# Kernel tuning notes

Hardware: AMD Instinct MI355X
Metric: run time of the kernel (lower is better)

Reference implementation:

```python
import jax, jax.numpy as jnp
import numpy as np

SOS_INDEX = 0


def setup_inputs() -> dict:
    key = jax.random.key(0)
    ks = jax.random.split(key, 12)
    T, B, H, V = 64, 1024, 512, 512
    s = 1.0 / np.sqrt(H)
    inp = {
        "target_var": jax.random.randint(ks[0], (T, B), 0, V, dtype=jnp.int64),
        "target_max_len": T,
        "encoder_hidden": jax.random.normal(ks[1], (B, H), jnp.float32),
        "encoder_cell": jax.random.normal(ks[2], (B, H), jnp.float32),
        "embedding": jax.random.normal(ks[3], (V, H), jnp.float32) * s,
        "W_ih": jax.random.normal(ks[4], (4 * H, H), jnp.float32) * s,
        "W_hh": jax.random.normal(ks[5], (4 * H, H), jnp.float32) * s,
        "b_ih": jax.random.normal(ks[6], (4 * H,), jnp.float32) * s,
        "b_hh": jax.random.normal(ks[7], (4 * H,), jnp.float32) * s,
        "W_out": jax.random.normal(ks[8], (V, H), jnp.float32) * s,
        "b_out": jax.random.normal(ks[9], (V,), jnp.float32) * s,
    }
    return inp


def reference(target_var, target_max_len, encoder_hidden, encoder_cell,
              embedding, W_ih, W_hh, b_ih, b_hh, W_out, b_out):
    B = target_var.shape[1]
    H = encoder_hidden.shape[1]
    # initial decoder input: embedding of SOS token for every batch element
    x0 = jnp.broadcast_to(embedding[SOS_INDEX], (B, H))
    bias = b_ih + b_hh  # [4H]

    def step(carry, _):
        x, h, c = carry
        # PyTorch LSTMCell: gate order i, f, g, o
        gates = x @ W_ih.T + h @ W_hh.T + bias  # [B, 4H]
        i, f, g, o = jnp.split(gates, 4, axis=-1)
        c_new = jax.nn.sigmoid(f) * c + jax.nn.sigmoid(i) * jnp.tanh(g)
        h_new = jax.nn.sigmoid(o) * jnp.tanh(c_new)
        logits = h_new @ W_out.T + b_out  # [B, V]
        # greedy decoding (topk(1)) -> next input embedding
        nxt = embedding[jnp.argmax(logits, axis=-1)]  # [B, H]
        return (nxt, h_new, c_new), logits

    _, outputs = jax.lax.scan(step, (x0, encoder_hidden, encoder_cell),
                              None, length=target_max_len)
    return outputs  # [T, B, V]
```

## Files before the change

kernel.cpp:

```cpp
#include <hip/hip_runtime.h>
#include <math.h>

constexpr int T_STEPS = 64;
constexpr int B_SZ = 1024;
constexpr int H_SZ = 512;
constexpr int V_SZ = 512;
constexpr int G_SZ = 4 * H_SZ;

typedef _Float16 half8 __attribute__((ext_vector_type(8)));
typedef _Float16 half4 __attribute__((ext_vector_type(4)));
typedef float f32x4 __attribute__((ext_vector_type(4)));

__device__ __forceinline__ float4 ld4(const float* p) {
    return *reinterpret_cast<const float4*>(p);
}
__device__ __forceinline__ void st4(float* p, float4 v) {
    *reinterpret_cast<float4*>(p) = v;
}
__device__ __forceinline__ float sigf(float x) { return 1.f / (1.f + expf(-x)); }

__device__ __forceinline__ unsigned long long pack_vc(float v, int col) {
    unsigned u = __float_as_uint(v);
    unsigned key = (u & 0x80000000u) ? ~u : (u | 0x80000000u);
    return ((unsigned long long)key << 32) | (unsigned)(511 - col);
}

__global__ __launch_bounds__(256) void cvt_pair(
    const float* __restrict__ x, _Float16* __restrict__ hi,
    _Float16* __restrict__ lo)
{
    const int i4 = blockIdx.x * 256 + threadIdx.x;
    const float4 v = ld4(x + (size_t)i4 * 4);
    half4 h, l;
    const float h0 = (float)(_Float16)v.x; h[0] = (_Float16)v.x; l[0] = (_Float16)((v.x - h0) * 2048.f);
    const float h1 = (float)(_Float16)v.y; h[1] = (_Float16)v.y; l[1] = (_Float16)((v.y - h1) * 2048.f);
    const float h2 = (float)(_Float16)v.z; h[2] = (_Float16)v.z; l[2] = (_Float16)((v.z - h2) * 2048.f);
    const float h3 = (float)(_Float16)v.w; h[3] = (_Float16)v.w; l[3] = (_Float16)((v.w - h3) * 2048.f);
    *reinterpret_cast<half4*>(hi + (size_t)i4 * 4) = h;
    *reinterpret_cast<half4*>(lo + (size_t)i4 * 4) = l;
}

__global__ __launch_bounds__(256) void gemm_nt_f32(
    const float* __restrict__ A, const float* __restrict__ Bw,
    float* __restrict__ C, int M, int N, int K,
    const float* __restrict__ bias1, const float* __restrict__ bias2)
{
    constexpr int BK = 16;
    __shared__ __align__(16) float As[BK][64];
    __shared__ __align__(16) float Bs[BK][64];
    const int tid = threadIdx.x;
    const int tx = tid % 16, ty = tid / 16;
    const int m0 = blockIdx.y * 64, n0 = blockIdx.x * 64;
    const int lr = tid / 4, lc = (tid % 4) * 4;
    float acc[4][4] = {};
    for (int k0 = 0; k0 < K; k0 += BK) {
        const float4 av = ld4(&A[(size_t)(m0 + lr) * K + (k0 + lc)]);
        const float4 bv = ld4(&Bw[(size_t)(n0 + lr) * K + (k0 + lc)]);
        __syncthreads();
        As[lc + 0][lr] = av.x; As[lc + 1][lr] = av.y; As[lc + 2][lr] = av.z; As[lc + 3][lr] = av.w;
        Bs[lc + 0][lr] = bv.x; Bs[lc + 1][lr] = bv.y; Bs[lc + 2][lr] = bv.z; Bs[lc + 3][lr] = bv.w;
        __syncthreads();
#pragma unroll
        for (int k = 0; k < BK; ++k) {
            const float4 a4 = ld4(&As[k][ty * 4]);
            const float4 b4 = ld4(&Bs[k][tx * 4]);
            const float ar[4] = {a4.x, a4.y, a4.z, a4.w};
            const float br[4] = {b4.x, b4.y, b4.z, b4.w};
#pragma unroll
            for (int i = 0; i < 4; ++i)
#pragma unroll
                for (int j = 0; j < 4; ++j)
                    acc[i][j] = fmaf(ar[i], br[j], acc[i][j]);
        }
    }
    const int nc = n0 + tx * 4;
    const float4 b1 = ld4(&bias1[nc]);
    const float4 b2 = ld4(&bias2[nc]);
#pragma unroll
    for (int i = 0; i < 4; ++i) {
        const int m = m0 + ty * 4 + i;
        float4 v;
        v.x = acc[i][0] + b1.x + b2.x; v.y = acc[i][1] + b1.y + b2.y;
        v.z = acc[i][2] + b1.z + b2.z; v.w = acc[i][3] + b1.w + b2.w;
        st4(&C[(size_t)m * N + nc], v);
    }
}

__global__ __launch_bounds__(256) void step_gates_cell(
    const _Float16* __restrict__ Ahi, const _Float16* __restrict__ Alo,
    const _Float16* __restrict__ Whh_hi, const _Float16* __restrict__ Whh_lo,
    const float* __restrict__ Eg,
    const unsigned long long* __restrict__ tok_cur,
    unsigned long long* __restrict__ tok_reset,
    float* __restrict__ cbuf,
    _Float16* __restrict__ Nhi, _Float16* __restrict__ Nlo)
{
    constexpr int LDK = 40;
    __shared__ __align__(16) char smem[64 * 129 * 4];
    _Float16* sAh = (_Float16*)smem;
    _Float16* sAl = sAh + 64 * LDK;
    _Float16* sBh = sAl + 64 * LDK;
    _Float16* sBl = sBh + 128 * LDK;
    float* sg = (float*)smem;

    const int tid = threadIdx.x;
    const int wave = tid >> 6, lane = tid & 63;
    const int wm = wave >> 1, wn = wave & 1;
    const int lm = lane & 15, kq = lane >> 4;
    const int h0 = blockIdx.x * 32;
    const int b0 = blockIdx.y * 64;

    const int ar = tid >> 2, akc = (tid & 3) * 8;
    const int r1 = tid >> 2, kc1 = (tid & 3) * 8;
    const int r2 = (tid + 256) >> 2, kc2 = kc1;
    const int g1 = (r1 >> 5) * 512 + h0 + (r1 & 31);
    const int g2 = (r2 >> 5) * 512 + h0 + (r2 & 31);

    const _Float16* pAh = Ahi + (size_t)(b0 + ar) * 512 + akc;
    const _Float16* pAl = Alo + (size_t)(b0 + ar) * 512 + akc;
    const _Float16* pB1h = Whh_hi + (size_t)g1 * 512 + kc1;
    const _Float16* pB1l = Whh_lo + (size_t)g1 * 512 + kc1;
    const _Float16* pB2h = Whh_hi + (size_t)g2 * 512 + kc2;
    const _Float16* pB2l = Whh_lo + (size_t)g2 * 512 + kc2;

    f32x4 aH[2][4] = {};
    f32x4 aC[2][4] = {};

    for (int k0 = 0; k0 < 512; k0 += 32) {
        const half8 va_h = *(const half8*)(pAh + k0);
        const half8 va_l = *(const half8*)(pAl + k0);
        const half8 vb1h = *(const half8*)(pB1h + k0);
        const half8 vb1l = *(const half8*)(pB1l + k0);
        const half8 vb2h = *(const half8*)(pB2h + k0);
        const half8 vb2l = *(const half8*)(pB2l + k0);
        __syncthreads();
        *(half8*)(sAh + ar * LDK + akc) = va_h;
        *(half8*)(sAl + ar * LDK + akc) = va_l;
        *(half8*)(sBh + r1 * LDK + kc1) = vb1h;
        *(half8*)(sBl + r1 * LDK + kc1) = vb1l;
        *(half8*)(sBh + r2 * LDK + kc2) = vb2h;
        *(half8*)(sBl + r2 * LDK + kc2) = vb2l;
        __syncthreads();

        half8 bh[4], bl[4];
#pragma unroll
        for (int gn = 0; gn < 4; ++gn) {
            const int rr = wn * 64 + gn * 16 + lm;
            bh[gn] = *(const half8*)(sBh + rr * LDK + kq * 8);
            bl[gn] = *(const half8*)(sBl + rr * LDK + kq * 8);
        }
#pragma unroll
        for (int gm = 0; gm < 2; ++gm) {
            const int rm = wm * 32 + gm * 16 + lm;
            const half8 ah = *(const half8*)(sAh + rm * LDK + kq * 8);
            const half8 al = *(const half8*)(sAl + rm * LDK + kq * 8);
#pragma unroll
            for (int gn = 0; gn < 4; ++gn)
                aH[gm][gn] = __builtin_amdgcn_mfma_f32_16x16x32_f16(ah, bh[gn], aH[gm][gn], 0, 0, 0);
#pragma unroll
            for (int gn = 0; gn < 4; ++gn)
                aC[gm][gn] = __builtin_amdgcn_mfma_f32_16x16x32_f16(ah, bl[gn], aC[gm][gn], 0, 0, 0);
#pragma unroll
            for (int gn = 0; gn < 4; ++gn)
                aC[gm][gn] = __builtin_amdgcn_mfma_f32_16x16x32_f16(al, bh[gn], aC[gm][gn], 0, 0, 0);
        }
    }

    __syncthreads();
#pragma unroll
    for (int gm = 0; gm < 2; ++gm) {
#pragma unroll
        for (int gn = 0; gn < 4; ++gn) {
            const int row = wm * 32 + gm * 16 + kq * 4;
            const int col = wn * 64 + gn * 16 + lm;
#pragma unroll
            for (int r = 0; r < 4; ++r)
                sg[(row + r) * 129 + col] =
                    aH[gm][gn][r] + aC[gm][gn][r] * (1.f / 2048.f);
        }
    }
    __syncthreads();

    const int crow = tid >> 2;
    const int hb = (tid & 3) * 8;
    const int b = b0 + crow;
    const unsigned long long pk = tok_cur[b];
    const int tk = 511 - (int)(unsigned)(pk & 0xFFFFFFFFu);
    const float* egp = Eg + (size_t)tk * G_SZ + h0;

#pragma unroll
    for (int q = 0; q < 2; ++q) {
        const int hh = hb + q * 4;
        const float* sr = sg + crow * 129;
        const float4 gI = ld4(sr + hh);
        const float4 gF = ld4(sr + 32 + hh);
        const float4 gG = ld4(sr + 64 + hh);
        const float4 gO = ld4(sr + 96 + hh);
        const float4 eI = ld4(egp + hh);
        const float4 eF = ld4(egp + 512 + hh);
        const float4 eG = ld4(egp + 1024 + hh);
        const float4 eO = ld4(egp + 1536 + hh);
        const size_t ci = (size_t)b * 512 + h0 + hh;
        const float4 cv = ld4(cbuf + ci);

        const float iv[4] = {gI.x + eI.x, gI.y + eI.y, gI.z + eI.z, gI.w + eI.w};
        const float fv[4] = {gF.x + eF.x, gF.y + eF.y, gF.z + eF.z, gF.w + eF.w};
        const float gv[4] = {gG.x + eG.x, gG.y + eG.y, gG.z + eG.z, gG.w + eG.w};
        const float ov[4] = {gO.x + eO.x, gO.y + eO.y, gO.z + eO.z, gO.w + eO.w};
        float cc[4] = {cv.x, cv.y, cv.z, cv.w};
        float hn[4];
#pragma unroll
        for (int j = 0; j < 4; ++j) {
            const float cn = sigf(fv[j]) * cc[j] + sigf(iv[j]) * tanhf(gv[j]);
            cc[j] = cn;
            hn[j] = sigf(ov[j]) * tanhf(cn);
        }
        st4(cbuf + ci, make_float4(cc[0], cc[1], cc[2], cc[3]));
        half4 h, l;
#pragma unroll
        for (int j = 0; j < 4; ++j) {
            const _Float16 hi = (_Float16)hn[j];
            h[j] = hi;
            l[j] = (_Float16)((hn[j] - (float)hi) * 2048.f);
        }
        *reinterpret_cast<half4*>(Nhi + ci) = h;
        *reinterpret_cast<half4*>(Nlo + ci) = l;
    }

    if (blockIdx.x == 0 && tid < 64) tok_reset[b0 + tid] = 0ULL;
}

__global__ __launch_bounds__(128) void step_logits_argmax(
    const _Float16* __restrict__ Ahi, const _Float16* __restrict__ Alo,
    const _Float16* __restrict__ Whi, const _Float16* __restrict__ Wlo,
    const float* __restrict__ b_out,
    float* __restrict__ outT,
    unsigned long long* __restrict__ tokmax)
{
    const int tid = threadIdx.x, wave = tid >> 6, lane = tid & 63;
    const int lm = lane & 15, kq = lane >> 4;
    const int n0 = blockIdx.x * 64;
    const int m0 = blockIdx.y * 32 + wave * 16;

    f32x4 aH[4] = {};
    f32x4 aC[4] = {};

    const _Float16* pAh = Ahi + (size_t)(m0 + lm) * 512 + kq * 8;
    const _Float16* pAl = Alo + (size_t)(m0 + lm) * 512 + kq * 8;

    for (int k0 = 0; k0 < 512; k0 += 32) {
        const half8 ah = *(const half8*)(pAh + k0);
        const half8 al = *(const half8*)(pAl + k0);
        half8 bh[4], bl[4];
#pragma unroll
        for (int gn = 0; gn < 4; ++gn) {
            const size_t off = (size_t)(n0 + gn * 16 + lm) * 512 + k0 + kq * 8;
            bh[gn] = *(const half8*)(Whi + off);
            bl[gn] = *(const half8*)(Wlo + off);
        }
#pragma unroll
        for (int gn = 0; gn < 4; ++gn)
            aH[gn] = __builtin_amdgcn_mfma_f32_16x16x32_f16(ah, bh[gn], aH[gn], 0, 0, 0);
#pragma unroll
        for (int gn = 0; gn < 4; ++gn)
            aC[gn] = __builtin_amdgcn_mfma_f32_16x16x32_f16(ah, bl[gn], aC[gn], 0, 0, 0);
#pragma unroll
        for (int gn = 0; gn < 4; ++gn)
            aC[gn] = __builtin_amdgcn_mfma_f32_16x16x32_f16(al, bh[gn], aC[gn], 0, 0, 0);
    }

    unsigned long long best[4] = {0ULL, 0ULL, 0ULL, 0ULL};
#pragma unroll
    for (int gn = 0; gn < 4; ++gn) {
        const int col = n0 + gn * 16 + lm;
        const float bo = b_out[col];
#pragma unroll
        for (int r = 0; r < 4; ++r) {
            const float v = aH[gn][r] + aC[gn][r] * (1.f / 2048.f) + bo;
            const int row = m0 + kq * 4 + r;
            outT[(size_t)row * V_SZ + col] = v;
            const unsigned long long p = pack_vc(v, col);
            if (p > best[r]) best[r] = p;
        }
    }
#pragma unroll
    for (int r = 0; r < 4; ++r) {
#pragma unroll
        for (int off = 1; off < 16; off <<= 1) {
            const unsigned long long o = __shfl_xor(best[r], off);
            if (o > best[r]) best[r] = o;
        }
    }
    if (lm == 0) {
#pragma unroll
        for (int r = 0; r < 4; ++r)
            atomicMax(&tokmax[m0 + kq * 4 + r], best[r]);
    }
}

__global__ __launch_bounds__(256) void init_tok(unsigned long long* __restrict__ tok)
{
    const int i = blockIdx.x * 256 + threadIdx.x;
    tok[i] = (i < 1024) ? 511ULL : 0ULL;
}

extern "C" void kernel_launch(void* const* d_in, const int* in_sizes, int n_in,
                              void* d_out, int out_size, void* d_ws, size_t ws_size,
                              hipStream_t stream)
{
    const float* enc_h = (const float*)d_in[2];
    const float* enc_c = (const float*)d_in[3];
    const float* emb   = (const float*)d_in[4];
    const float* W_ih  = (const float*)d_in[5];
    const float* W_hh  = (const float*)d_in[6];
    const float* b_ih  = (const float*)d_in[7];
    const float* b_hh  = (const float*)d_in[8];
    const float* W_out = (const float*)d_in[9];
    const float* b_out = (const float*)d_in[10];
    float* out = (float*)d_out;

    char* ws = (char*)d_ws;
    _Float16* Whh_hi  = (_Float16*)(ws);
    _Float16* Whh_lo  = (_Float16*)(ws + (2u << 20));
    _Float16* Wout_hi = (_Float16*)(ws + (4u << 20));
    _Float16* Wout_lo = (_Float16*)(ws + (4u << 20) + (512u << 10));
    _Float16* Hhi[2] = {(_Float16*)(ws + (5u << 20)), (_Float16*)(ws + (7u << 20))};
    _Float16* Hlo[2] = {(_Float16*)(ws + (6u << 20)), (_Float16*)(ws + (8u << 20))};
    float* cbuf = (float*)(ws + (9u << 20));
    float* Eg   = (float*)(ws + (11u << 20));
    unsigned long long* tokbuf = (unsigned long long*)(ws + (15u << 20));

    const dim3 blk256(256), blk128(128);

    cvt_pair<<<(G_SZ * H_SZ) / 1024, blk256, 0, stream>>>(W_hh, Whh_hi, Whh_lo);
    cvt_pair<<<(V_SZ * H_SZ) / 1024, blk256, 0, stream>>>(W_out, Wout_hi, Wout_lo);
    cvt_pair<<<(B_SZ * H_SZ) / 1024, blk256, 0, stream>>>(enc_h, Hhi[0], Hlo[0]);
    hipMemcpyAsync(cbuf, enc_c, (size_t)B_SZ * H_SZ * 4, hipMemcpyDeviceToDevice, stream);
    init_tok<<<8, blk256, 0, stream>>>(tokbuf);

    gemm_nt_f32<<<dim3(G_SZ / 64, V_SZ / 64), blk256, 0, stream>>>(
        emb, W_ih, Eg, V_SZ, G_SZ, H_SZ, b_ih, b_hh);

    for (int t = 0; t < T_STEPS; ++t) {
        const int cur = t & 1, nxt = (t + 1) & 1;
        step_gates_cell<<<dim3(H_SZ / 32, B_SZ / 64), blk256, 0, stream>>>(
            Hhi[cur], Hlo[cur], Whh_hi, Whh_lo, Eg,
            tokbuf + cur * B_SZ, tokbuf + nxt * B_SZ,
            cbuf, Hhi[nxt], Hlo[nxt]);

        step_logits_argmax<<<dim3(V_SZ / 64, B_SZ / 32), blk128, 0, stream>>>(
            Hhi[nxt], Hlo[nxt], Wout_hi, Wout_lo, b_out,
            out + (size_t)t * B_SZ * V_SZ, tokbuf + nxt * B_SZ);
    }
}
```

Baseline: 2.302 ms.

## Fuse per-step decoder kernels into one persistent kernel with grid barriers

```diff
diff --git a/kernel.cpp b/kernel.cpp
--- a/kernel.cpp
+++ b/kernel.cpp
@@ -6,6 +6,7 @@
 constexpr int H_SZ = 512;
 constexpr int V_SZ = 512;
 constexpr int G_SZ = 4 * H_SZ;
+constexpr int N_BLOCKS = 256;
 
 typedef _Float16 half8 __attribute__((ext_vector_type(8)));
 typedef _Float16 half4 __attribute__((ext_vector_type(4)));
@@ -23,6 +24,27 @@
     unsigned u = __float_as_uint(v);
     unsigned key = (u & 0x80000000u) ? ~u : (u | 0x80000000u);
     return ((unsigned long long)key << 32) | (unsigned)(511 - col);
+}
+
+__device__ __forceinline__ void grid_barrier(unsigned* cnt, unsigned* gen) {
+    __syncthreads();
+    if (threadIdx.x == 0) {
+        const unsigned g = __hip_atomic_load(gen, __ATOMIC_RELAXED,
+                                             __HIP_MEMORY_SCOPE_AGENT);
+        const unsigned arrived = __hip_atomic_fetch_add(
+            cnt, 1u, __ATOMIC_ACQ_REL, __HIP_MEMORY_SCOPE_AGENT) + 1u;
+        if (arrived == (unsigned)N_BLOCKS) {
+            __hip_atomic_store(cnt, 0u, __ATOMIC_RELAXED,
+                               __HIP_MEMORY_SCOPE_AGENT);
+            __hip_atomic_fetch_add(gen, 1u, __ATOMIC_RELEASE,
+                                   __HIP_MEMORY_SCOPE_AGENT);
+        } else {
+            while (__hip_atomic_load(gen, __ATOMIC_ACQUIRE,
+                                     __HIP_MEMORY_SCOPE_AGENT) == g)
+                __builtin_amdgcn_s_sleep(2);
+        }
+    }
+    __syncthreads();
 }
 
 __global__ __launch_bounds__(256) void cvt_pair(
@@ -86,14 +108,22 @@
     }
 }
 
-__global__ __launch_bounds__(256) void step_gates_cell(
-    const _Float16* __restrict__ Ahi, const _Float16* __restrict__ Alo,
+__global__ __launch_bounds__(256) void init_state(
+    unsigned long long* __restrict__ tok, unsigned* __restrict__ bar)
+{
+    const int i = blockIdx.x * 256 + threadIdx.x;
+    tok[i] = (i < 1024) ? 511ULL : 0ULL;
+    if (i < 2) bar[i] = 0u;
+}
+
+__global__ __launch_bounds__(256, 1) void persistent_decoder(
     const _Float16* __restrict__ Whh_hi, const _Float16* __restrict__ Whh_lo,
-    const float* __restrict__ Eg,
-    const unsigned long long* __restrict__ tok_cur,
-    unsigned long long* __restrict__ tok_reset,
-    float* __restrict__ cbuf,
-    _Float16* __restrict__ Nhi, _Float16* __restrict__ Nlo)
+    const _Float16* __restrict__ Wout_hi, const _Float16* __restrict__ Wout_lo,
+    const float* __restrict__ Eg, const float* __restrict__ b_out,
+    _Float16* __restrict__ H0hi, _Float16* __restrict__ H0lo,
+    _Float16* __restrict__ H1hi, _Float16* __restrict__ H1lo,
+    float* __restrict__ cbuf, unsigned long long* __restrict__ tokbuf,
+    unsigned* __restrict__ bar, float* __restrict__ out)
 {
     constexpr int LDK = 40;
     __shared__ __align__(16) char smem[64 * 129 * 4];
@@ -103,205 +133,215 @@
     _Float16* sBl = sBh + 128 * LDK;
     float* sg = (float*)smem;
 
+    unsigned* bar_cnt = bar;
+    unsigned* bar_gen = bar + 1;
+
+    const int bid = blockIdx.x;
     const int tid = threadIdx.x;
     const int wave = tid >> 6, lane = tid & 63;
+    const int lm = lane & 15, kq = lane >> 4;
+
     const int wm = wave >> 1, wn = wave & 1;
-    const int lm = lane & 15, kq = lane >> 4;
-    const int h0 = blockIdx.x * 32;
-    const int b0 = blockIdx.y * 64;
-
+    const int h0 = (bid & 15) * 32;
+    const int b0 = (bid >> 4) * 64;
     const int ar = tid >> 2, akc = (tid & 3) * 8;
-    const int r1 = tid >> 2, kc1 = (tid & 3) * 8;
-    const int r2 = (tid + 256) >> 2, kc2 = kc1;
-    const int g1 = (r1 >> 5) * 512 + h0 + (r1 & 31);
+    const int r2 = ar + 64;
+    const int g1 = (ar >> 5) * 512 + h0 + (ar & 31);
     const int g2 = (r2 >> 5) * 512 + h0 + (r2 & 31);
-
-    const _Float16* pAh = Ahi + (size_t)(b0 + ar) * 512 + akc;
-    const _Float16* pAl = Alo + (size_t)(b0 + ar) * 512 + akc;
-    const _Float16* pB1h = Whh_hi + (size_t)g1 * 512 + kc1;
-    const _Float16* pB1l = Whh_lo + (size_t)g1 * 512 + kc1;
-    const _Float16* pB2h = Whh_hi + (size_t)g2 * 512 + kc2;
-    const _Float16* pB2l = Whh_lo + (size_t)g2 * 512 + kc2;
-
-    f32x4 aH[2][4] = {};
-    f32x4 aC[2][4] = {};
-
-    for (int k0 = 0; k0 < 512; k0 += 32) {
-        const half8 va_h = *(const half8*)(pAh + k0);
-        const half8 va_l = *(const half8*)(pAl + k0);
-        const half8 vb1h = *(const half8*)(pB1h + k0);
-        const half8 vb1l = *(const half8*)(pB1l + k0);
-        const half8 vb2h = *(const half8*)(pB2h + k0);
-        const half8 vb2l = *(const half8*)(pB2l + k0);
-        __syncthreads();
-        *(half8*)(sAh + ar * LDK + akc) = va_h;
-        *(half8*)(sAl + ar * LDK + akc) = va_l;
-        *(half8*)(sBh + r1 * LDK + kc1) = vb1h;
-        *(half8*)(sBl + r1 * LDK + kc1) = vb1l;
-        *(half8*)(sBh + r2 * LDK + kc2) = vb2h;
-        *(half8*)(sBl + r2 * LDK + kc2) = vb2l;
-        __syncthreads();
-
-        half8 bh[4], bl[4];
-#pragma unroll
-        for (int gn = 0; gn < 4; ++gn) {
-            const int rr = wn * 64 + gn * 16 + lm;
-            bh[gn] = *(const half8*)(sBh + rr * LDK + kq * 8);
-            bl[gn] = *(const half8*)(sBl + rr * LDK + kq * 8);
-        }
-#pragma unroll
-        for (int gm = 0; gm < 2; ++gm) {
-            const int rm = wm * 32 + gm * 16 + lm;
-            const half8 ah = *(const half8*)(sAh + rm * LDK + kq * 8);
-            const half8 al = *(const half8*)(sAl + rm * LDK + kq * 8);
-#pragma unroll
-            for (int gn = 0; gn < 4; ++gn)
-                aH[gm][gn] = __builtin_amdgcn_mfma_f32_16x16x32_f16(ah, bh[gn], aH[gm][gn], 0, 0, 0);
-#pragma unroll
-            for (int gn = 0; gn < 4; ++gn)
-                aC[gm][gn] = __builtin_amdgcn_mfma_f32_16x16x32_f16(ah, bl[gn], aC[gm][gn], 0, 0, 0);
-#pragma unroll
-            for (int gn = 0; gn < 4; ++gn)
-                aC[gm][gn] = __builtin_amdgcn_mfma_f32_16x16x32_f16(al, bh[gn], aC[gm][gn], 0, 0, 0);
-        }
-    }
-
-    __syncthreads();
-#pragma unroll
-    for (int gm = 0; gm < 2; ++gm) {
-#pragma unroll
-        for (int gn = 0; gn < 4; ++gn) {
-            const int row = wm * 32 + gm * 16 + kq * 4;
-            const int col = wn * 64 + gn * 16 + lm;
-#pragma unroll
-            for (int r = 0; r < 4; ++r)
-                sg[(row + r) * 129 + col] =
-                    aH[gm][gn][r] + aC[gm][gn][r] * (1.f / 2048.f);
-        }
-    }
-    __syncthreads();
-
+    const _Float16* pB1h = Whh_hi + (size_t)g1 * 512 + akc;
+    const _Float16* pB1l = Whh_lo + (size_t)g1 * 512 + akc;
+    const _Float16* pB2h = Whh_hi + (size_t)g2 * 512 + akc;
+    const _Float16* pB2l = Whh_lo + (size_t)g2 * 512 + akc;
     const int crow = tid >> 2;
     const int hb = (tid & 3) * 8;
-    const int b = b0 + crow;
-    const unsigned long long pk = tok_cur[b];
-    const int tk = 511 - (int)(unsigned)(pk & 0xFFFFFFFFu);
-    const float* egp = Eg + (size_t)tk * G_SZ + h0;
-
-#pragma unroll
-    for (int q = 0; q < 2; ++q) {
-        const int hh = hb + q * 4;
-        const float* sr = sg + crow * 129;
-        const float4 gI = ld4(sr + hh);
-        const float4 gF = ld4(sr + 32 + hh);
-        const float4 gG = ld4(sr + 64 + hh);
-        const float4 gO = ld4(sr + 96 + hh);
-        const float4 eI = ld4(egp + hh);
-        const float4 eF = ld4(egp + 512 + hh);
-        const float4 eG = ld4(egp + 1024 + hh);
-        const float4 eO = ld4(egp + 1536 + hh);
-        const size_t ci = (size_t)b * 512 + h0 + hh;
-        const float4 cv = ld4(cbuf + ci);
-
-        const float iv[4] = {gI.x + eI.x, gI.y + eI.y, gI.z + eI.z, gI.w + eI.w};
-        const float fv[4] = {gF.x + eF.x, gF.y + eF.y, gF.z + eF.z, gF.w + eF.w};
-        const float gv[4] = {gG.x + eG.x, gG.y + eG.y, gG.z + eG.z, gG.w + eG.w};
-        const float ov[4] = {gO.x + eO.x, gO.y + eO.y, gO.z + eO.z, gO.w + eO.w};
-        float cc[4] = {cv.x, cv.y, cv.z, cv.w};
-        float hn[4];
-#pragma unroll
-        for (int j = 0; j < 4; ++j) {
-            const float cn = sigf(fv[j]) * cc[j] + sigf(iv[j]) * tanhf(gv[j]);
-            cc[j] = cn;
-            hn[j] = sigf(ov[j]) * tanhf(cn);
+
+    const int wm2 = wave >> 1, wn2 = wave & 1;
+    const int m0_2 = (bid >> 3) * 32 + wm2 * 16;
+    const int n0_2 = (bid & 7) * 64 + wn2 * 32;
+    const size_t wo0 = (size_t)(n0_2 + lm) * 512 + kq * 8;
+    const size_t wo1 = (size_t)(n0_2 + 16 + lm) * 512 + kq * 8;
+    const float bo0 = b_out[n0_2 + lm];
+    const float bo1 = b_out[n0_2 + 16 + lm];
+
+    for (int t = 0; t < T_STEPS; ++t) {
+        const _Float16* Ahi = (t & 1) ? H1hi : H0hi;
+        const _Float16* Alo = (t & 1) ? H1lo : H0lo;
+        _Float16* Nhi = (t & 1) ? H0hi : H1hi;
+        _Float16* Nlo = (t & 1) ? H0lo : H1lo;
+        const unsigned long long* tok_cur = tokbuf + (t & 1) * B_SZ;
+        unsigned long long* tok_nxt = tokbuf + ((t + 1) & 1) * B_SZ;
+
+        {
+            const _Float16* pAh = Ahi + (size_t)(b0 + ar) * 512 + akc;
+            const _Float16* pAl = Alo + (size_t)(b0 + ar) * 512 + akc;
+            f32x4 aH[2][4] = {};
+            f32x4 aC[2][4] = {};
+            half8 va_h = *(const half8*)(pAh);
+            half8 va_l = *(const half8*)(pAl);
+            half8 vb1h = *(const half8*)(pB1h);
+            half8 vb1l = *(const half8*)(pB1l);
+            half8 vb2h = *(const half8*)(pB2h);
+            half8 vb2l = *(const half8*)(pB2l);
+
+            for (int it = 0; it < 16; ++it) {
+                __syncthreads();
+                *(half8*)(sAh + ar * LDK + akc) = va_h;
+                *(half8*)(sAl + ar * LDK + akc) = va_l;
+                *(half8*)(sBh + ar * LDK + akc) = vb1h;
+                *(half8*)(sBl + ar * LDK + akc) = vb1l;
+                *(half8*)(sBh + r2 * LDK + akc) = vb2h;
+                *(half8*)(sBl + r2 * LDK + akc) = vb2l;
+                __syncthreads();
+
+                const int kn = ((it + 1) & 15) * 32;
+                va_h = *(const half8*)(pAh + kn);
+                va_l = *(const half8*)(pAl + kn);
+                vb1h = *(const half8*)(pB1h + kn);
+                vb1l = *(const half8*)(pB1l + kn);
+                vb2h = *(const half8*)(pB2h + kn);
+                vb2l = *(const half8*)(pB2l + kn);
+
+                half8 bh[4], bl[4];
+#pragma unroll
+                for (int gn = 0; gn < 4; ++gn) {
+                    const int rr = wn * 64 + gn * 16 + lm;
+                    bh[gn] = *(const half8*)(sBh + rr * LDK + kq * 8);
+                    bl[gn] = *(const half8*)(sBl + rr * LDK + kq * 8);
+                }
+#pragma unroll
+                for (int gm = 0; gm < 2; ++gm) {
+                    const int rm = wm * 32 + gm * 16 + lm;
+                    const half8 ah = *(const half8*)(sAh + rm * LDK + kq * 8);
+                    const half8 al = *(const half8*)(sAl + rm * LDK + kq * 8);
+#pragma unroll
+                    for (int gn = 0; gn < 4; ++gn)
+                        aH[gm][gn] = __builtin_amdgcn_mfma_f32_16x16x32_f16(ah, bh[gn], aH[gm][gn], 0, 0, 0);
+#pragma unroll
+                    for (int gn = 0; gn < 4; ++gn)
+                        aC[gm][gn] = __builtin_amdgcn_mfma_f32_16x16x32_f16(ah, bl[gn], aC[gm][gn], 0, 0, 0);
+#pragma unroll
+                    for (int gn = 0; gn < 4; ++gn)
+                        aC[gm][gn] = __builtin_amdgcn_mfma_f32_16x16x32_f16(al, bh[gn], aC[gm][gn], 0, 0, 0);
+                }
+            }
+
+            __syncthreads();
+#pragma unroll
+            for (int gm = 0; gm < 2; ++gm) {
+#pragma unroll
+                for (int gn = 0; gn < 4; ++gn) {
+                    const int row = wm * 32 + gm * 16 + kq * 4;
+                    const int col = wn * 64 + gn * 16 + lm;
+#pragma unroll
+                    for (int r = 0; r < 4; ++r)
+                        sg[(row + r) * 129 + col] =
+                            aH[gm][gn][r] + aC[gm][gn][r] * (1.f / 2048.f);
+                }
+            }
+            __syncthreads();
+
+            const int b = b0 + crow;
+            const unsigned long long pk = tok_cur[b];
+            const int tk = 511 - (int)(unsigned)(pk & 0xFFFFFFFFu);
+            const float* egp = Eg + (size_t)tk * G_SZ + h0;
+
+#pragma unroll
+            for (int q = 0; q < 2; ++q) {
+                const int hh = hb + q * 4;
+                const float* sr = sg + crow * 129;
+                const float4 gI = ld4(sr + hh);
+                const float4 gF = ld4(sr + 32 + hh);
+                const float4 gG = ld4(sr + 64 + hh);
+                const float4 gO = ld4(sr + 96 + hh);
+                const float4 eI = ld4(egp + hh);
+                const float4 eF = ld4(egp + 512 + hh);
+                const float4 eG = ld4(egp + 1024 + hh);
+                const float4 eO = ld4(egp + 1536 + hh);
+                const size_t ci = (size_t)b * 512 + h0 + hh;
+                const float4 cv = ld4(cbuf + ci);
+
+                const float iv[4] = {gI.x + eI.x, gI.y + eI.y, gI.z + eI.z, gI.w + eI.w};
+                const float fv[4] = {gF.x + eF.x, gF.y + eF.y, gF.z + eF.z, gF.w + eF.w};
+                const float gv[4] = {gG.x + eG.x, gG.y + eG.y, gG.z + eG.z, gG.w + eG.w};
+                const float ov[4] = {gO.x + eO.x, gO.y + eO.y, gO.z + eO.z, gO.w + eO.w};
+                float cc[4] = {cv.x, cv.y, cv.z, cv.w};
+                float hn[4];
+#pragma unroll
+                for (int j = 0; j < 4; ++j) {
+                    const float cn = sigf(fv[j]) * cc[j] + sigf(iv[j]) * tanhf(gv[j]);
+                    cc[j] = cn;
+                    hn[j] = sigf(ov[j]) * tanhf(cn);
+                }
+                st4(cbuf + ci, make_float4(cc[0], cc[1], cc[2], cc[3]));
+                half4 h, l;
+#pragma unroll
+                for (int j = 0; j < 4; ++j) {
+                    const _Float16 hi = (_Float16)hn[j];
+                    h[j] = hi;
+                    l[j] = (_Float16)((hn[j] - (float)hi) * 2048.f);
+                }
+                *reinterpret_cast<half4*>(Nhi + ci) = h;
+                *reinterpret_cast<half4*>(Nlo + ci) = l;
+            }
+
+            if ((bid & 15) == 0 && tid < 64) tok_nxt[b0 + tid] = 0ULL;
         }
-        st4(cbuf + ci, make_float4(cc[0], cc[1], cc[2], cc[3]));
-        half4 h, l;
-#pragma unroll
-        for (int j = 0; j < 4; ++j) {
-            const _Float16 hi = (_Float16)hn[j];
-            h[j] = hi;
-            l[j] = (_Float16)((hn[j] - (float)hi) * 2048.f);
+
+        grid_barrier(bar_cnt, bar_gen);
+
+        {
+            f32x4 aH[2] = {};
+            f32x4 aC[2] = {};
+            const _Float16* pA2h = Nhi + (size_t)(m0_2 + lm) * 512 + kq * 8;
+            const _Float16* pA2l = Nlo + (size_t)(m0_2 + lm) * 512 + kq * 8;
+#pragma unroll 2
+            for (int k0 = 0; k0 < 512; k0 += 32) {
+                const half8 ah = *(const half8*)(pA2h + k0);
+                const half8 al = *(const half8*)(pA2l + k0);
+                const half8 b0h = *(const half8*)(Wout_hi + wo0 + k0);
+                const half8 b0l = *(const half8*)(Wout_lo + wo0 + k0);
+                const half8 b1h = *(const half8*)(Wout_hi + wo1 + k0);
+                const half8 b1l = *(const half8*)(Wout_lo + wo1 + k0);
+                aH[0] = __builtin_amdgcn_mfma_f32_16x16x32_f16(ah, b0h, aH[0], 0, 0, 0);
+                aH[1] = __builtin_amdgcn_mfma_f32_16x16x32_f16(ah, b1h, aH[1], 0, 0, 0);
+                aC[0] = __builtin_amdgcn_mfma_f32_16x16x32_f16(ah, b0l, aC[0], 0, 0, 0);
+                aC[1] = __builtin_amdgcn_mfma_f32_16x16x32_f16(ah, b1l, aC[1], 0, 0, 0);
+                aC[0] = __builtin_amdgcn_mfma_f32_16x16x32_f16(al, b0h, aC[0], 0, 0, 0);
+                aC[1] = __builtin_amdgcn_mfma_f32_16x16x32_f16(al, b1h, aC[1], 0, 0, 0);
+            }
+
+            float* outT = out + (size_t)t * B_SZ * V_SZ;
+            unsigned long long best[4] = {0ULL, 0ULL, 0ULL, 0ULL};
+#pragma unroll
+            for (int gn = 0; gn < 2; ++gn) {
+                const int col = n0_2 + gn * 16 + lm;
+                const float bo = gn ? bo1 : bo0;
+#pragma unroll
+                for (int r = 0; r < 4; ++r) {
+                    const float v = aH[gn][r] + aC[gn][r] * (1.f / 2048.f) + bo;
+                    const int row = m0_2 + kq * 4 + r;
+                    __builtin_nontemporal_store(v, &outT[(size_t)row * V_SZ + col]);
+                    const unsigned long long p = pack_vc(v, col);
+                    if (p > best[r]) best[r] = p;
+                }
+            }
+#pragma unroll
+            for (int r = 0; r < 4; ++r) {
+#pragma unroll
+                for (int off = 1; off < 16; off <<= 1) {
+                    const unsigned long long o = __shfl_xor(best[r], off);
+                    if (o > best[r]) best[r] = o;
+                }
+            }
+            if (lm == 0) {
+#pragma unroll
+                for (int r = 0; r < 4; ++r)
+                    atomicMax(&tok_nxt[m0_2 + kq * 4 + r], best[r]);
+            }
         }
-        *reinterpret_cast<half4*>(Nhi + ci) = h;
-        *reinterpret_cast<half4*>(Nlo + ci) = l;
+
+        grid_barrier(bar_cnt, bar_gen);
     }
-
-    if (blockIdx.x == 0 && tid < 64) tok_reset[b0 + tid] = 0ULL;
-}
-
-__global__ __launch_bounds__(128) void step_logits_argmax(
-    const _Float16* __restrict__ Ahi, const _Float16* __restrict__ Alo,
-    const _Float16* __restrict__ Whi, const _Float16* __restrict__ Wlo,
-    const float* __restrict__ b_out,
-    float* __restrict__ outT,
-    unsigned long long* __restrict__ tokmax)
-{
-    const int tid = threadIdx.x, wave = tid >> 6, lane = tid & 63;
-    const int lm = lane & 15, kq = lane >> 4;
-    const int n0 = blockIdx.x * 64;
-    const int m0 = blockIdx.y * 32 + wave * 16;
-
-    f32x4 aH[4] = {};
-    f32x4 aC[4] = {};
-
-    const _Float16* pAh = Ahi + (size_t)(m0 + lm) * 512 + kq * 8;
-    const _Float16* pAl = Alo + (size_t)(m0 + lm) * 512 + kq * 8;
-
-    for (int k0 = 0; k0 < 512; k0 += 32) {
-        const half8 ah = *(const half8*)(pAh + k0);
-        const half8 al = *(const half8*)(pAl + k0);
-        half8 bh[4], bl[4];
-#pragma unroll
-        for (int gn = 0; gn < 4; ++gn) {
-            const size_t off = (size_t)(n0 + gn * 16 + lm) * 512 + k0 + kq * 8;
-            bh[gn] = *(const half8*)(Whi + off);
-            bl[gn] = *(const half8*)(Wlo + off);
-        }
-#pragma unroll
-        for (int gn = 0; gn < 4; ++gn)
-            aH[gn] = __builtin_amdgcn_mfma_f32_16x16x32_f16(ah, bh[gn], aH[gn], 0, 0, 0);
-#pragma unroll
-        for (int gn = 0; gn < 4; ++gn)
-            aC[gn] = __builtin_amdgcn_mfma_f32_16x16x32_f16(ah, bl[gn], aC[gn], 0, 0, 0);
-#pragma unroll
-        for (int gn = 0; gn < 4; ++gn)
-            aC[gn] = __builtin_amdgcn_mfma_f32_16x16x32_f16(al, bh[gn], aC[gn], 0, 0, 0);
-    }
-
-    unsigned long long best[4] = {0ULL, 0ULL, 0ULL, 0ULL};
-#pragma unroll
-    for (int gn = 0; gn < 4; ++gn) {
-        const int col = n0 + gn * 16 + lm;
-        const float bo = b_out[col];
-#pragma unroll
-        for (int r = 0; r < 4; ++r) {
-            const float v = aH[gn][r] + aC[gn][r] * (1.f / 2048.f) + bo;
-            const int row = m0 + kq * 4 + r;
-            outT[(size_t)row * V_SZ + col] = v;
-            const unsigned long long p = pack_vc(v, col);
-            if (p > best[r]) best[r] = p;
-        }
-    }
-#pragma unroll
-    for (int r = 0; r < 4; ++r) {
-#pragma unroll
-        for (int off = 1; off < 16; off <<= 1) {
-            const unsigned long long o = __shfl_xor(best[r], off);
-            if (o > best[r]) best[r] = o;
-        }
-    }
-    if (lm == 0) {
-#pragma unroll
-        for (int r = 0; r < 4; ++r)
-            atomicMax(&tokmax[m0 + kq * 4 + r], best[r]);
-    }
-}
-
-__global__ __launch_bounds__(256) void init_tok(unsigned long long* __restrict__ tok)
-{
-    const int i = blockIdx.x * 256 + threadIdx.x;
-    tok[i] = (i < 1024) ? 511ULL : 0ULL;
 }
 
 extern "C" void kernel_launch(void* const* d_in, const int* in_sizes, int n_in,
@@ -324,32 +364,27 @@
     _Float16* Whh_lo  = (_Float16*)(ws + (2u << 20));
     _Float16* Wout_hi = (_Float16*)(ws + (4u << 20));
     _Float16* Wout_lo = (_Float16*)(ws + (4u << 20) + (512u << 10));
-    _Float16* Hhi[2] = {(_Float16*)(ws + (5u << 20)), (_Float16*)(ws + (7u << 20))};
-    _Float16* Hlo[2] = {(_Float16*)(ws + (6u << 20)), (_Float16*)(ws + (8u << 20))};
+    _Float16* H0hi = (_Float16*)(ws + (5u << 20));
+    _Float16* H0lo = (_Float16*)(ws + (6u << 20));
+    _Float16* H1hi = (_Float16*)(ws + (7u << 20));
+    _Float16* H1lo = (_Float16*)(ws + (8u << 20));
     float* cbuf = (float*)(ws + (9u << 20));
     float* Eg   = (float*)(ws + (11u << 20));
     unsigned long long* tokbuf = (unsigned long long*)(ws + (15u << 20));
-
-    const dim3 blk256(256), blk128(128);
+    unsigned* bar = (unsigned*)(ws + (15u << 20) + (64u << 10));
+
+    const dim3 blk256(256);
 
     cvt_pair<<<(G_SZ * H_SZ) / 1024, blk256, 0, stream>>>(W_hh, Whh_hi, Whh_lo);
     cvt_pair<<<(V_SZ * H_SZ) / 1024, blk256, 0, stream>>>(W_out, Wout_hi, Wout_lo);
-    cvt_pair<<<(B_SZ * H_SZ) / 1024, blk256, 0, stream>>>(enc_h, Hhi[0], Hlo[0]);
+    cvt_pair<<<(B_SZ * H_SZ) / 1024, blk256, 0, stream>>>(enc_h, H0hi, H0lo);
     hipMemcpyAsync(cbuf, enc_c, (size_t)B_SZ * H_SZ * 4, hipMemcpyDeviceToDevice, stream);
-    init_tok<<<8, blk256, 0, stream>>>(tokbuf);
+    init_state<<<8, blk256, 0, stream>>>(tokbuf, bar);
 
     gemm_nt_f32<<<dim3(G_SZ / 64, V_SZ / 64), blk256, 0, stream>>>(
         emb, W_ih, Eg, V_SZ, G_SZ, H_SZ, b_ih, b_hh);
 
-    for (int t = 0; t < T_STEPS; ++t) {
-        const int cur = t & 1, nxt = (t + 1) & 1;
-        step_gates_cell<<<dim3(H_SZ / 32, B_SZ / 64), blk256, 0, stream>>>(
-            Hhi[cur], Hlo[cur], Whh_hi, Whh_lo, Eg,
-            tokbuf + cur * B_SZ, tokbuf + nxt * B_SZ,
-            cbuf, Hhi[nxt], Hlo[nxt]);
-
-        step_logits_argmax<<<dim3(V_SZ / 64, B_SZ / 32), blk128, 0, stream>>>(
-            Hhi[nxt], Hlo[nxt], Wout_hi, Wout_lo, b_out,
-            out + (size_t)t * B_SZ * V_SZ, tokbuf + nxt * B_SZ);
-    }
-}
+    persistent_decoder<<<dim3(N_BLOCKS), blk256, 0, stream>>>(
+        Whh_hi, Whh_lo, Wout_hi, Wout_lo, Eg, b_out,
+        H0hi, H0lo, H1hi, H1lo, cbuf, tokbuf, bar, out);
+}
```

Result: slower. 5.355 ms (+132.6%).
